# Optimization experiments

Measured on AMD Instinct MI355X. Metric: run time of the kernel, lower is better.

Reference implementation:

```python
import jax, jax.numpy as jnp
import numpy as np

D_MODEL = 768
N_HEADS = 12

def setup_inputs() -> dict:
    key = jax.random.key(0)
    ks = jax.random.split(key, 5)
    D = D_MODEL
    x = jax.random.normal(ks[0], (2, 4096, D), dtype=jnp.float32)
    s_attn = 1.0 / np.sqrt(D)
    s_proj = 1.0 / np.sqrt(D)
    W_attn = jax.random.uniform(ks[1], (D, 3 * D), minval=-s_attn, maxval=s_attn, dtype=jnp.float32)
    b_attn = jax.random.uniform(ks[2], (3 * D,), minval=-s_attn, maxval=s_attn, dtype=jnp.float32)
    W_proj = jax.random.uniform(ks[3], (D, D), minval=-s_proj, maxval=s_proj, dtype=jnp.float32)
    b_proj = jax.random.uniform(ks[4], (D,), minval=-s_proj, maxval=s_proj, dtype=jnp.float32)
    return {"x": x, "W_attn": W_attn, "b_attn": b_attn, "W_proj": W_proj, "b_proj": b_proj}

def reference(x, W_attn, b_attn, W_proj, b_proj):
    B, T, C = x.shape
    H = N_HEADS
    hd = C // H
    qkv = x @ W_attn + b_attn                     # [B,T,3C]
    q, k, v = jnp.split(qkv, 3, axis=-1)
    # [B,T,C] -> [B,H,T,hd]
    q = q.reshape(B, T, H, hd).transpose(0, 2, 1, 3)
    k = k.reshape(B, T, H, hd).transpose(0, 2, 1, 3)
    v = v.reshape(B, T, H, hd).transpose(0, 2, 1, 3)
    att = jnp.einsum('bhqd,bhkd->bhqk', q, k) * (1.0 / np.sqrt(hd))
    causal = jnp.tril(jnp.ones((T, T), dtype=bool))
    att = jnp.where(causal, att, -jnp.inf)
    att = jax.nn.softmax(att, axis=-1)
    y = jnp.einsum('bhqk,bhkd->bhqd', att, v)     # [B,H,T,hd]
    y = y.transpose(0, 2, 1, 3).reshape(B, T, C)
    return y @ W_proj + b_proj
```

## Files before the change

kernel.cpp:

```cpp
#include <hip/hip_runtime.h>
#include <hip/hip_bf16.h>

typedef __attribute__((ext_vector_type(8))) short bf16x8;
typedef __attribute__((ext_vector_type(4))) float f32x4;
typedef __attribute__((ext_vector_type(16))) float f32x16;
typedef __attribute__((ext_vector_type(4))) int i32x4;

#define DEVI __device__ __forceinline__

namespace {
constexpr int BATCH = 2;
constexpr int T = 4096;
constexpr int C = 768;
constexpr int H = 12;
constexpr int HD = 64;
constexpr int M = BATCH * T;
constexpr int N3 = 3 * C;
constexpr int BH = BATCH * H;
constexpr float QSCALE = 0.125f * 1.44269504088896f;
constexpr int PSZ = 64 * 128 + 128;
}

DEVI ushort f2b(float f) {
  union { float f; unsigned u; } v; v.f = f;
  unsigned r = (v.u + 0x7FFFu + ((v.u >> 16) & 1u)) >> 16;
  return (ushort)r;
}

DEVI f32x16 zero16() {
  f32x16 z;
#pragma unroll
  for (int i = 0; i < 16; i++) z[i] = 0.f;
  return z;
}

DEVI void gload16(const void* g, void* l) {
  __builtin_amdgcn_global_load_lds(
      (const __attribute__((address_space(1))) unsigned int*)g,
      (__attribute__((address_space(3))) unsigned int*)l, 16, 0, 0);
}

__global__ __launch_bounds__(256) void cvt_kernel(const float* __restrict__ src,
                                                  ushort* __restrict__ dst, int n) {
  int i = (blockIdx.x * 256 + threadIdx.x) * 4;
  int stride = gridDim.x * 256 * 4;
  for (; i < n; i += stride) {
    float4 v = *reinterpret_cast<const float4*>(src + i);
    ushort4 o;
    o.x = f2b(v.x); o.y = f2b(v.y); o.z = f2b(v.z); o.w = f2b(v.w);
    *reinterpret_cast<ushort4*>(dst + i) = o;
  }
}

__global__ __launch_bounds__(256) void cvtT_kernel(const float* __restrict__ src,
                                                   ushort* __restrict__ dst,
                                                   int K, int N) {
  __shared__ ushort Lt[64 * 68];
  const int k0 = blockIdx.x * 64, n0 = blockIdx.y * 64;
  const int tid = threadIdx.x;
  const int rr = tid >> 4, c4 = (tid & 15) * 4;
#pragma unroll
  for (int it = 0; it < 4; it++) {
    const int r = it * 16 + rr;
    float4 v = *reinterpret_cast<const float4*>(src + (size_t)(k0 + r) * N + n0 + c4);
    Lt[(c4 + 0) * 68 + r] = f2b(v.x);
    Lt[(c4 + 1) * 68 + r] = f2b(v.y);
    Lt[(c4 + 2) * 68 + r] = f2b(v.z);
    Lt[(c4 + 3) * 68 + r] = f2b(v.w);
  }
  __syncthreads();
#pragma unroll
  for (int it = 0; it < 4; it++) {
    const int r = it * 16 + rr;
    *reinterpret_cast<ushort4*>(dst + (size_t)(n0 + r) * K + k0 + c4) =
        *reinterpret_cast<const ushort4*>(&Lt[r * 68 + c4]);
  }
}

template <int EPI>
__global__ __launch_bounds__(256, 3) void gemm_kernel(
    const ushort* __restrict__ A, const ushort* __restrict__ Bt,
    const float* __restrict__ bias, int N, int Kd,
    ushort* __restrict__ qo, ushort* __restrict__ ko, ushort* __restrict__ vo,
    float* __restrict__ fo) {
  constexpr int BM = 128;
  constexpr int BN = 128;
  constexpr int WN = 2;
  constexpr int WTN = BN / WN;
  constexpr int NT = WTN / 32;
  constexpr int CH_A = BM / 8;
  constexpr int CH_B = BN / 8;
  constexpr int CPW = (CH_A + CH_B) / 4;
  constexpr int SMEM = (EPI == 0) ? (4 * 64 * 68) : ((BM + BN) * 64);
  __shared__ ushort smem[SMEM];
  ushort* As = smem;
  ushort* Bs = smem + BM * 64;

  const int tid = threadIdx.x;
  const int lane = tid & 63;
  const int w = tid >> 6;
  const int l31 = lane & 31;
  const int hi = lane >> 5;
  const int wm = w / WN, wn = w % WN;
  const int m0 = blockIdx.y * BM, n0 = blockIdx.x * BN;
  const int r8 = lane >> 3, c8 = lane & 7;
  const int csw = (c8 ^ r8) * 8;

  f32x16 acc[2][NT];
#pragma unroll
  for (int mt = 0; mt < 2; mt++)
#pragma unroll
    for (int nt = 0; nt < NT; nt++) acc[mt][nt] = zero16();

  for (int k0 = 0; k0 < Kd; k0 += 64) {
    __syncthreads();
#pragma unroll
    for (int ci = 0; ci < CPW; ci++) {
      const int chk = w * CPW + ci;
      if (chk < CH_A) {
        gload16(A + (size_t)(m0 + chk * 8 + r8) * Kd + k0 + csw, (char*)As + chk * 1024);
      } else {
        const int ch2 = chk - CH_A;
        gload16(Bt + (size_t)(n0 + ch2 * 8 + r8) * Kd + k0 + csw, (char*)Bs + ch2 * 1024);
      }
    }
    __syncthreads();
#pragma unroll
    for (int ks = 0; ks < 4; ks++) {
      bf16x8 af[2], bf[NT];
#pragma unroll
      for (int mt = 0; mt < 2; mt++) {
        const int rl = wm * 64 + mt * 32 + l31;
        af[mt] = *reinterpret_cast<const bf16x8*>(
            &As[rl * 64 + ((ks * 16 + hi * 8) ^ ((rl & 7) * 8))]);
      }
#pragma unroll
      for (int nt = 0; nt < NT; nt++) {
        const int nl = wn * WTN + nt * 32 + l31;
        bf[nt] = *reinterpret_cast<const bf16x8*>(
            &Bs[nl * 64 + ((ks * 16 + hi * 8) ^ ((nl & 7) * 8))]);
      }
#pragma unroll
      for (int mt = 0; mt < 2; mt++)
#pragma unroll
        for (int nt = 0; nt < NT; nt++)
          acc[mt][nt] = __builtin_amdgcn_mfma_f32_32x32x16_bf16(af[mt], bf[nt], acc[mt][nt], 0, 0, 0);
    }
  }

  if constexpr (EPI == 0) {
    if (n0 >= 1536) {
      __syncthreads();
      ushort* Vw = smem + w * 4352;
      const float bv0 = bias[n0 + wn * 64 + l31];
      const float bv1 = bias[n0 + wn * 64 + 32 + l31];
#pragma unroll
      for (int mt = 0; mt < 2; mt++)
#pragma unroll
        for (int nt = 0; nt < 2; nt++) {
          const float bv = nt ? bv1 : bv0;
#pragma unroll
          for (int r = 0; r < 16; r++) {
            const int trow = mt * 32 + (r & 3) + ((r >> 2) << 3) + (hi << 2);
            Vw[(nt * 32 + l31) * 68 + trow] = f2b(acc[mt][nt][r] + bv);
          }
        }
      const int hh = (n0 - 1536) / 64 + wn;
      const int bb = m0 >> 12;
      const int t0 = (m0 & (T - 1)) + wm * 64;
      const size_t vbase = (size_t)((bb * H + hh) * 64 + lane) * T + t0;
#pragma unroll
      for (int x8 = 0; x8 < 8; x8++) {
        bf16x8 vv = *reinterpret_cast<const bf16x8*>(&Vw[lane * 68 + x8 * 8]);
        *reinterpret_cast<bf16x8*>(vo + vbase + ((x8 ^ (lane & 7)) * 8)) = vv;
      }
    } else {
#pragma unroll
      for (int mt = 0; mt < 2; mt++)
#pragma unroll
        for (int nt = 0; nt < 2; nt++) {
          const int n = n0 + wn * 64 + nt * 32 + l31;
          const float bv = bias[n];
          const int part = (n >= 768) ? 1 : 0;
          const int ci = n - part * 768;
          const int hh = ci >> 6, dd = ci & 63;
#pragma unroll
          for (int r = 0; r < 16; r++) {
            const int m = m0 + wm * 64 + mt * 32 + (r & 3) + ((r >> 2) << 3) + (hi << 2);
            const int bb = m >> 12, t = m & (T - 1);
            const float val = acc[mt][nt][r] + bv;
            if (part == 0) {
              qo[((size_t)(bb * H + hh) * T + t) * HD + dd] = f2b(val * QSCALE);
            } else {
              ko[((size_t)(bb * H + hh) * T + t) * HD + (dd ^ ((t & 7) << 3))] = f2b(val);
            }
          }
        }
    }
  } else {
#pragma unroll
    for (int mt = 0; mt < 2; mt++)
#pragma unroll
      for (int nt = 0; nt < NT; nt++) {
        const int n = n0 + wn * WTN + nt * 32 + l31;
        const float bv = bias[n];
#pragma unroll
        for (int r = 0; r < 16; r++) {
          const int m = m0 + wm * 64 + mt * 32 + (r & 3) + ((r >> 2) << 3) + (hi << 2);
          fo[(size_t)m * N + n] = acc[mt][nt][r] + bv;
        }
      }
  }
}

__global__ __launch_bounds__(256, 3) void attn_kernel(
    const ushort* __restrict__ Qg, const ushort* __restrict__ Kg,
    const ushort* __restrict__ Vtg, ushort* __restrict__ Yg,
    float* __restrict__ Pp) {
  __shared__ ushort kbuf[128 * 64];
  __shared__ ushort vbuf[2 * 2 * 64 * 64];

  const int tid = threadIdx.x;
  const int lane = tid & 63;
  const int w = tid >> 6;
  const int l31 = lane & 31;
  const int hi = lane >> 5;
  const int r8 = lane >> 3, c8 = lane & 7;

  const int bid = blockIdx.x;
  const int xcd = bid & 7, idx = bid >> 3;
  const int bh = xcd * 3 + idx % 3;
  const int slot = idx / 3;

  int qtA, qtB, kvbase, bnd, ntot, pA, pB;
  if (slot < 8) {
    qtA = slot; qtB = 15 - slot; kvbase = 0; bnd = slot + 1; ntot = 17; pA = -1; pB = -1;
  } else if (slot < 24) {
    qtA = slot + 8; qtB = -1; kvbase = 0; bnd = 100; ntot = 16;
    pA = (bh * 16 + (qtA - 16)) * 2; pB = -1;
  } else {
    const int a = slot - 24;
    qtA = 16 + a; qtB = 31 - a; kvbase = 16; bnd = a + 1; ntot = 17;
    pA = (bh * 16 + a) * 2 + 1; pB = (bh * 16 + (15 - a)) * 2 + 1;
  }

  const int bb = bh / H, h = bh % H;
  const ushort* Qp = Qg + (size_t)bh * T * HD;
  const char* Kbp = (const char*)(Kg + (size_t)bh * T * HD);
  const char* Vbp = (const char*)(Vtg + (size_t)bh * HD * T);

  bf16x8 qcur[4];
#pragma unroll
  for (int ks = 0; ks < 4; ks++)
    qcur[ks] = *reinterpret_cast<const bf16x8*>(
        Qp + (size_t)(qtA * 128 + w * 32 + l31) * HD + ks * 16 + hi * 8);

  int q0 = qtA * 128, q0w = q0 + w * 32, qc = q0w + l31;
  int pcur = pA;

  const f32x16 ZF = zero16();

  f32x16 o16[2];
  o16[0] = zero16();
  o16[1] = zero16();
  float sa = 0.f, sb = 0.f, sc = 0.f, sd = 0.f;
  const int swz = (l31 & 7) << 3;

  auto kvt_of = [&](int tt) { return kvbase + (tt < bnd ? tt : tt - bnd); };

  auto issue_K = [&](int kvt) {
    const int kv0 = kvt * 128;
#pragma unroll
    for (int c2 = 0; c2 < 4; c2++) {
      const int chk = w * 4 + c2;
      gload16(Kbp + ((size_t)(kv0 + chk * 8 + r8) * 64 + c8 * 8) * 2,
              (char*)kbuf + chk * 1024);
    }
  };
  auto issue_V = [&](int kvt, int par) {
    const int kv0 = kvt * 128;
#pragma unroll
    for (int c2 = 0; c2 < 4; c2++) {
      const int chk = w * 4 + c2;
      const int st = chk >> 3;
      const int d8 = chk & 7;
      gload16(Vbp + ((size_t)(d8 * 8 + r8) * T + kv0 + st * 64 + c8 * 8) * 2,
              (char*)vbuf + par * 16384 + chk * 1024);
    }
  };

  auto epilogue = [&](int q0p, float lr, ushort* Ytb) {
    ushort* Yw = Ytb + w * 1152;
    const float linv = 1.0f / lr;
#pragma unroll
    for (int dt = 0; dt < 2; dt++) {
#pragma unroll
      for (int r = 0; r < 16; r++) {
        const int d32 = (r & 3) + ((r >> 2) << 3) + (hi << 2);
        Yw[l31 * 36 + d32] = f2b(o16[dt][r] * linv);
      }
#pragma unroll
      for (int seg = 0; seg < 2; seg++) {
        bf16x8 vv = *reinterpret_cast<const bf16x8*>(&Yw[l31 * 36 + hi * 16 + seg * 8]);
        *reinterpret_cast<bf16x8*>(
            Yg + ((size_t)(bb * T + q0p + w * 32 + l31)) * C + h * 64 + dt * 32 +
            hi * 16 + seg * 8) = vv;
      }
    }
  };

  auto pwrite = [&](float* P, float lr) {
#pragma unroll
    for (int dt = 0; dt < 2; dt++)
#pragma unroll
      for (int r = 0; r < 16; r++) {
        const int d = dt * 32 + (r & 3) + ((r >> 2) << 3) + (hi << 2);
        P[d * 128 + w * 32 + l31] = o16[dt][r];
      }
    P[8192 + w * 32 + l31] = lr;
  };

  issue_K(kvt_of(0));
  issue_V(kvt_of(0), 0);

  for (int tt = 0; tt < ntot; tt++) {
    asm volatile("s_waitcnt vmcnt(0)" ::: "memory");
    __builtin_amdgcn_s_barrier();
    __builtin_amdgcn_sched_barrier(0);

    if (tt == bnd) {
      float lr = (sa + sb) + (sc + sd);
      lr += __shfl_xor(lr, 32);
      if (pcur >= 0) pwrite(Pp + (size_t)pcur * PSZ, lr);
      else epilogue(q0, lr, vbuf + ((tt + 1) & 1) * 8192);
      o16[0] = zero16(); o16[1] = zero16();
      sa = sb = sc = sd = 0.f;
#pragma unroll
      for (int ks = 0; ks < 4; ks++)
        qcur[ks] = *reinterpret_cast<const bf16x8*>(
            Qp + (size_t)(qtB * 128 + w * 32 + l31) * HD + ks * 16 + hi * 8);
      q0 = qtB * 128; q0w = q0 + w * 32; qc = q0w + l31; pcur = pB;
    }

    const int kvt = kvt_of(tt);
    const int kv0 = kvt * 128;
    bool have[4], needm[4];
#pragma unroll
    for (int sub = 0; sub < 4; sub++) {
      have[sub] = (kv0 + sub * 32) <= (q0w + 31);
      needm[sub] = (kv0 + sub * 32 + 31) > q0w;
    }

    f32x16 s2[4];
#pragma unroll
    for (int sub = 0; sub < 4; sub++) {
      if (!have[sub]) continue;
      const int row = sub * 32 + l31;
      __builtin_amdgcn_s_setprio(1);
      bf16x8 kf = *reinterpret_cast<const bf16x8*>(&kbuf[row * 64 + ((hi * 8) ^ swz)]);
      f32x16 acc = __builtin_amdgcn_mfma_f32_32x32x16_bf16(kf, qcur[0], ZF, 0, 0, 0);
#pragma unroll
      for (int ks = 1; ks < 4; ks++) {
        kf = *reinterpret_cast<const bf16x8*>(
            &kbuf[row * 64 + ((ks * 16 + hi * 8) ^ swz)]);
        acc = __builtin_amdgcn_mfma_f32_32x32x16_bf16(kf, qcur[ks], acc, 0, 0, 0);
      }
      __builtin_amdgcn_s_setprio(0);
      if (needm[sub]) {
#pragma unroll
        for (int r2 = 0; r2 < 16; r2++) {
          const int kv = kv0 + sub * 32 + (r2 & 3) + ((r2 >> 2) << 3) + (hi << 2);
          if (kv > qc) acc[r2] = -1e30f;
        }
      }
      s2[sub] = acc;
    }

    asm volatile("s_waitcnt lgkmcnt(0)" ::: "memory");
    __builtin_amdgcn_s_barrier();
    __builtin_amdgcn_sched_barrier(0);
    if (tt + 1 < ntot) {
      const int nkvt = kvt_of(tt + 1);
      issue_K(nkvt);
      issue_V(nkvt, (tt + 1) & 1);
    }

#pragma unroll
    for (int sub = 0; sub < 4; sub++) {
      if (!have[sub]) continue;
#pragma unroll
      for (int r2 = 0; r2 < 16; r2 += 4) {
        s2[sub][r2]     = __builtin_amdgcn_exp2f(s2[sub][r2]);     sa += s2[sub][r2];
        s2[sub][r2 + 1] = __builtin_amdgcn_exp2f(s2[sub][r2 + 1]); sb += s2[sub][r2 + 1];
        s2[sub][r2 + 2] = __builtin_amdgcn_exp2f(s2[sub][r2 + 2]); sc += s2[sub][r2 + 2];
        s2[sub][r2 + 3] = __builtin_amdgcn_exp2f(s2[sub][r2 + 3]); sd += s2[sub][r2 + 3];
      }
    }

    const ushort* Vpar = vbuf + (tt & 1) * 8192;
#pragma unroll
    for (int sub = 0; sub < 4; sub++) {
      if (!have[sub]) continue;
      const ushort* Vst = Vpar + (sub >> 1) * 4096;
      const int colb = (sub & 1) * 32;
#pragma unroll
      for (int ks2 = 0; ks2 < 2; ks2++) {
        const int r0 = ks2 * 8;
        int a0, a1, b0, b1;
        asm("v_cvt_pk_bf16_f32 %0, %1, %2" : "=v"(a0) : "v"(s2[sub][r0 + 0]), "v"(s2[sub][r0 + 1]));
        asm("v_cvt_pk_bf16_f32 %0, %1, %2" : "=v"(a1) : "v"(s2[sub][r0 + 2]), "v"(s2[sub][r0 + 3]));
        asm("v_cvt_pk_bf16_f32 %0, %1, %2" : "=v"(b0) : "v"(s2[sub][r0 + 4]), "v"(s2[sub][r0 + 5]));
        asm("v_cvt_pk_bf16_f32 %0, %1, %2" : "=v"(b1) : "v"(s2[sub][r0 + 6]), "v"(s2[sub][r0 + 7]));
        asm("v_permlane32_swap_b32 %0, %1" : "+v"(a0), "+v"(b0));
        asm("v_permlane32_swap_b32 %0, %1" : "+v"(a1), "+v"(b1));
        const i32x4 pi = {a0, a1, b0, b1};
        const bf16x8 pf = __builtin_bit_cast(bf16x8, pi);
        __builtin_amdgcn_s_setprio(1);
#pragma unroll
        for (int dt = 0; dt < 2; dt++) {
          const int drow = dt * 32 + l31;
          const int sw2 = (drow & 7) << 3;
          bf16x8 vf = *reinterpret_cast<const bf16x8*>(
              &Vst[drow * 64 + ((colb + ks2 * 16 + hi * 8) ^ sw2)]);
          o16[dt] = __builtin_amdgcn_mfma_f32_32x32x16_bf16(vf, pf, o16[dt], 0, 0, 0);
        }
        __builtin_amdgcn_s_setprio(0);
      }
    }
  }

  {
    float lr = (sa + sb) + (sc + sd);
    lr += __shfl_xor(lr, 32);
    if (pcur >= 0) pwrite(Pp + (size_t)pcur * PSZ, lr);
    else epilogue(q0, lr, vbuf + (ntot & 1) * 8192);
  }
}

__global__ __launch_bounds__(128) void combine_kernel(const float* __restrict__ Pp,
                                                      ushort* __restrict__ Yg) {
  __shared__ ushort Yt[128 * 68];
  const int bid = blockIdx.x;
  const int bh = bid >> 4, qq = bid & 15;
  const int bb = bh / H, h = bh % H;
  const int q0 = (16 + qq) * 128;
  const int q = threadIdx.x;
  const float* P1 = Pp + (size_t)(bh * 16 + qq) * 2 * PSZ;
  const float* P2 = P1 + PSZ;
  const float inv = 1.0f / (P1[8192 + q] + P2[8192 + q]);
#pragma unroll 8
  for (int d = 0; d < 64; d++)
    Yt[q * 68 + d] = f2b((P1[d * 128 + q] + P2[d * 128 + q]) * inv);
  __syncthreads();
#pragma unroll
  for (int it = 0; it < 2; it++) {
    const int row = it * 64 + (q >> 1), half = q & 1;
#pragma unroll
    for (int seg = 0; seg < 4; seg++) {
      bf16x8 vv = *reinterpret_cast<const bf16x8*>(&Yt[row * 68 + half * 32 + seg * 8]);
      *reinterpret_cast<bf16x8*>(
          Yg + ((size_t)(bb * T + q0 + row)) * C + h * 64 + half * 32 + seg * 8) = vv;
    }
  }
}

extern "C" void kernel_launch(void* const* d_in, const int* in_sizes, int n_in,
                              void* d_out, int out_size, void* d_ws, size_t ws_size,
                              hipStream_t stream) {
  const float* x = (const float*)d_in[0];
  const float* Wa = (const float*)d_in[1];
  const float* ba = (const float*)d_in[2];
  const float* Wp = (const float*)d_in[3];
  const float* bp = (const float*)d_in[4];
  float* out = (float*)d_out;

  char* ws = (char*)d_ws;
  size_t off = 0;
  auto carve = [&](size_t bytes) {
    void* p = ws + off;
    off += (bytes + 255) & ~(size_t)255;
    return p;
  };
  ushort* xb   = (ushort*)carve((size_t)M * C * 2);
  ushort* WaT  = (ushort*)carve((size_t)N3 * C * 2);
  ushort* WpT  = (ushort*)carve((size_t)C * C * 2);
  ushort* Qb   = (ushort*)carve((size_t)BH * T * HD * 2);
  ushort* Kb   = (ushort*)carve((size_t)BH * T * HD * 2);
  ushort* Vtb  = (ushort*)carve((size_t)BH * HD * T * 2);
  ushort* Yb   = (ushort*)carve((size_t)M * C * 2);
  float*  Pp   = (float*)carve((size_t)BH * 16 * 2 * PSZ * 4);

  cvt_kernel<<<2048, 256, 0, stream>>>(x, xb, M * C);
  cvtT_kernel<<<dim3(C / 64, N3 / 64), 256, 0, stream>>>(Wa, WaT, C, N3);
  cvtT_kernel<<<dim3(C / 64, C / 64), 256, 0, stream>>>(Wp, WpT, C, C);

  gemm_kernel<0><<<dim3(N3 / 128, M / 128), 256, 0, stream>>>(
      xb, WaT, ba, N3, C, Qb, Kb, Vtb, nullptr);

  attn_kernel<<<dim3(768), 256, 0, stream>>>(Qb, Kb, Vtb, Yb, Pp);
  combine_kernel<<<dim3(BH * 16), 128, 0, stream>>>(Pp, Yb);

  gemm_kernel<1><<<dim3(C / 128, M / 128), 256, 0, stream>>>(
      Yb, WpT, bp, C, C, nullptr, nullptr, nullptr, out);
}
```

Measured before the change: 168.0 us.

## Stage Q/K epilogue through LDS, store partials in bf16, shrink proj GEMM tile

The QKV GEMM epilogue for Q and K now writes through a per-wave LDS tile and emits 16-byte vector stores, replacing scattered 2-byte stores. This is meant to cut the uncoalesced global write cost. Split-KV attention partial outputs are now stored in bf16 with a separate fp32 row-sum array, which halves the traffic into the combine kernel at some precision cost. The output projection GEMM uses 64x128 tiles with four column warps, doubling its block count to fill more CUs.

Measured after the change: 170.2 us. Within noise of the previous version (+1.4%).

```diff
diff --git a/kernel.cpp b/kernel.cpp
--- a/kernel.cpp
+++ b/kernel.cpp
@@ -18,13 +18,18 @@
 constexpr int N3 = 3 * C;
 constexpr int BH = BATCH * H;
 constexpr float QSCALE = 0.125f * 1.44269504088896f;
-constexpr int PSZ = 64 * 128 + 128;
+constexpr int POSZ = 64 * 128;
 }
 
 DEVI ushort f2b(float f) {
   union { float f; unsigned u; } v; v.f = f;
   unsigned r = (v.u + 0x7FFFu + ((v.u >> 16) & 1u)) >> 16;
   return (ushort)r;
+}
+
+DEVI float b2f(ushort u) {
+  union { unsigned u; float f; } v; v.u = ((unsigned)u) << 16;
+  return v.f;
 }
 
 DEVI f32x16 zero16() {
@@ -83,9 +88,9 @@
     const float* __restrict__ bias, int N, int Kd,
     ushort* __restrict__ qo, ushort* __restrict__ ko, ushort* __restrict__ vo,
     float* __restrict__ fo) {
-  constexpr int BM = 128;
+  constexpr int BM = (EPI == 0) ? 128 : 64;
   constexpr int BN = 128;
-  constexpr int WN = 2;
+  constexpr int WN = (EPI == 0) ? 2 : 4;
   constexpr int WTN = BN / WN;
   constexpr int NT = WTN / 32;
   constexpr int CH_A = BM / 8;
@@ -165,6 +170,7 @@
             Vw[(nt * 32 + l31) * 68 + trow] = f2b(acc[mt][nt][r] + bv);
           }
         }
+      __syncthreads();
       const int hh = (n0 - 1536) / 64 + wn;
       const int bb = m0 >> 12;
       const int t0 = (m0 & (T - 1)) + wm * 64;
@@ -175,27 +181,37 @@
         *reinterpret_cast<bf16x8*>(vo + vbase + ((x8 ^ (lane & 7)) * 8)) = vv;
       }
     } else {
+      __syncthreads();
+      ushort* Lw = smem + w * 4352;
+      const int n_abs = n0 + wn * 64;
+      const bool isQ = (n_abs < 768);
+      const int hh = (n_abs - (isQ ? 0 : 768)) >> 6;
+      const float bv0 = bias[n_abs + l31];
+      const float bv1 = bias[n_abs + 32 + l31];
 #pragma unroll
       for (int mt = 0; mt < 2; mt++)
 #pragma unroll
         for (int nt = 0; nt < 2; nt++) {
-          const int n = n0 + wn * 64 + nt * 32 + l31;
-          const float bv = bias[n];
-          const int part = (n >= 768) ? 1 : 0;
-          const int ci = n - part * 768;
-          const int hh = ci >> 6, dd = ci & 63;
+          const float bv = nt ? bv1 : bv0;
 #pragma unroll
           for (int r = 0; r < 16; r++) {
-            const int m = m0 + wm * 64 + mt * 32 + (r & 3) + ((r >> 2) << 3) + (hi << 2);
-            const int bb = m >> 12, t = m & (T - 1);
-            const float val = acc[mt][nt][r] + bv;
-            if (part == 0) {
-              qo[((size_t)(bb * H + hh) * T + t) * HD + dd] = f2b(val * QSCALE);
-            } else {
-              ko[((size_t)(bb * H + hh) * T + t) * HD + (dd ^ ((t & 7) << 3))] = f2b(val);
-            }
+            const int trow = mt * 32 + (r & 3) + ((r >> 2) << 3) + (hi << 2);
+            float val = acc[mt][nt][r] + bv;
+            if (isQ) val *= QSCALE;
+            Lw[trow * 68 + nt * 32 + l31] = f2b(val);
           }
         }
+      __syncthreads();
+      const int bb = m0 >> 12;
+      const int t = (m0 & (T - 1)) + wm * 64 + lane;
+      const size_t base = ((size_t)(bb * H + hh) * T + t) * 64;
+      ushort* dst = isQ ? qo : ko;
+      const int lsw = isQ ? 0 : (lane & 7);
+#pragma unroll
+      for (int x8 = 0; x8 < 8; x8++) {
+        bf16x8 vv = *reinterpret_cast<const bf16x8*>(&Lw[lane * 68 + x8 * 8]);
+        *reinterpret_cast<bf16x8*>(dst + base + ((x8 ^ lsw) * 8)) = vv;
+      }
     }
   } else {
 #pragma unroll
@@ -216,7 +232,7 @@
 __global__ __launch_bounds__(256, 3) void attn_kernel(
     const ushort* __restrict__ Qg, const ushort* __restrict__ Kg,
     const ushort* __restrict__ Vtg, ushort* __restrict__ Yg,
-    float* __restrict__ Pp) {
+    ushort* __restrict__ Po, float* __restrict__ Pl) {
   __shared__ ushort kbuf[128 * 64];
   __shared__ ushort vbuf[2 * 2 * 64 * 64];
 
@@ -309,15 +325,16 @@
     }
   };
 
-  auto pwrite = [&](float* P, float lr) {
+  auto pwrite = [&](int pi, float lr) {
+    ushort* P = Po + (size_t)pi * POSZ;
 #pragma unroll
     for (int dt = 0; dt < 2; dt++)
 #pragma unroll
       for (int r = 0; r < 16; r++) {
         const int d = dt * 32 + (r & 3) + ((r >> 2) << 3) + (hi << 2);
-        P[d * 128 + w * 32 + l31] = o16[dt][r];
-      }
-    P[8192 + w * 32 + l31] = lr;
+        P[d * 128 + w * 32 + l31] = f2b(o16[dt][r]);
+      }
+    Pl[pi * 128 + w * 32 + l31] = lr;
   };
 
   issue_K(kvt_of(0));
@@ -331,7 +348,7 @@
     if (tt == bnd) {
       float lr = (sa + sb) + (sc + sd);
       lr += __shfl_xor(lr, 32);
-      if (pcur >= 0) pwrite(Pp + (size_t)pcur * PSZ, lr);
+      if (pcur >= 0) pwrite(pcur, lr);
       else epilogue(q0, lr, vbuf + ((tt + 1) & 1) * 8192);
       o16[0] = zero16(); o16[1] = zero16();
       sa = sb = sc = sd = 0.f;
@@ -432,12 +449,13 @@
   {
     float lr = (sa + sb) + (sc + sd);
     lr += __shfl_xor(lr, 32);
-    if (pcur >= 0) pwrite(Pp + (size_t)pcur * PSZ, lr);
+    if (pcur >= 0) pwrite(pcur, lr);
     else epilogue(q0, lr, vbuf + (ntot & 1) * 8192);
   }
 }
 
-__global__ __launch_bounds__(128) void combine_kernel(const float* __restrict__ Pp,
+__global__ __launch_bounds__(128) void combine_kernel(const ushort* __restrict__ Po,
+                                                      const float* __restrict__ Pl,
                                                       ushort* __restrict__ Yg) {
   __shared__ ushort Yt[128 * 68];
   const int bid = blockIdx.x;
@@ -445,12 +463,13 @@
   const int bb = bh / H, h = bh % H;
   const int q0 = (16 + qq) * 128;
   const int q = threadIdx.x;
-  const float* P1 = Pp + (size_t)(bh * 16 + qq) * 2 * PSZ;
-  const float* P2 = P1 + PSZ;
-  const float inv = 1.0f / (P1[8192 + q] + P2[8192 + q]);
+  const int pi = (bh * 16 + qq) * 2;
+  const ushort* P1 = Po + (size_t)pi * POSZ;
+  const ushort* P2 = P1 + POSZ;
+  const float inv = 1.0f / (Pl[pi * 128 + q] + Pl[pi * 128 + 128 + q]);
 #pragma unroll 8
   for (int d = 0; d < 64; d++)
-    Yt[q * 68 + d] = f2b((P1[d * 128 + q] + P2[d * 128 + q]) * inv);
+    Yt[q * 68 + d] = f2b((b2f(P1[d * 128 + q]) + b2f(P2[d * 128 + q])) * inv);
   __syncthreads();
 #pragma unroll
   for (int it = 0; it < 2; it++) {
@@ -488,7 +507,8 @@
   ushort* Kb   = (ushort*)carve((size_t)BH * T * HD * 2);
   ushort* Vtb  = (ushort*)carve((size_t)BH * HD * T * 2);
   ushort* Yb   = (ushort*)carve((size_t)M * C * 2);
-  float*  Pp   = (float*)carve((size_t)BH * 16 * 2 * PSZ * 4);
+  ushort* Po   = (ushort*)carve((size_t)BH * 16 * 2 * POSZ * 2);
+  float*  Pl   = (float*)carve((size_t)BH * 16 * 2 * 128 * 4);
 
   cvt_kernel<<<2048, 256, 0, stream>>>(x, xb, M * C);
   cvtT_kernel<<<dim3(C / 64, N3 / 64), 256, 0, stream>>>(Wa, WaT, C, N3);
@@ -497,9 +517,9 @@
   gemm_kernel<0><<<dim3(N3 / 128, M / 128), 256, 0, stream>>>(
       xb, WaT, ba, N3, C, Qb, Kb, Vtb, nullptr);
 
-  attn_kernel<<<dim3(768), 256, 0, stream>>>(Qb, Kb, Vtb, Yb, Pp);
-  combine_kernel<<<dim3(BH * 16), 128, 0, stream>>>(Pp, Yb);
-
-  gemm_kernel<1><<<dim3(C / 128, M / 128), 256, 0, stream>>>(
+  attn_kernel<<<dim3(768), 256, 0, stream>>>(Qb, Kb, Vtb, Yb, Po, Pl);
+  combine_kernel<<<dim3(BH * 16), 128, 0, stream>>>(Po, Pl, Yb);
+
+  gemm_kernel<1><<<dim3(C / 128, M / 64), 256, 0, stream>>>(
       Yb, WpT, bp, C, C, nullptr, nullptr, nullptr, out);
 }
```
